# Performance work log

Hardware: AMD Instinct MI355X
Metric: run time of the kernel (lower is better)

## Reference

```python
import jax, jax.numpy as jnp
import numpy as np

# norse LIFParameters defaults
ALPHA = 100.0        # superspike surrogate slope
DT = 1e-3
TAU_SYN_INV = 200.0  # 1/5e-3
TAU_MEM_INV = 100.0  # 1/1e-2
V_TH = 1.0           # v_leak = v_reset = 0

@jax.custom_vjp
def heaviside(v):
    # forward: hard threshold; backward: superspike surrogate 1/(alpha*|v|+1)^2
    return (v > 0).astype(v.dtype)

def _hv_fwd(v):
    return heaviside(v), v

def _hv_bwd(v, g):
    return (g / (ALPHA * jnp.abs(v) + 1.0) ** 2,)

heaviside.defvjp(_hv_fwd, _hv_bwd)

def setup_inputs() -> dict:
    key = jax.random.key(0)
    ks = jax.random.split(key, 5)
    B, H, W, O = 2048, 15, 15, 10
    x = jax.random.uniform(ks[0], (B, 1, H, W), jnp.float32)  # image-like in [0,1)
    conv_w = jax.random.normal(ks[1], (2, 1, 4, 4), jnp.float32) * 0.25
    conv_b = jax.random.normal(ks[2], (2,), jnp.float32) * 0.1
    lin_w = jax.random.normal(ks[3], (O, 72), jnp.float32) * (1.0 / np.sqrt(72.0))
    lin_b = jax.random.normal(ks[4], (O,), jnp.float32) * 0.1
    return {"x": x, "conv_w": conv_w, "conv_b": conv_b,
            "lin_w": lin_w, "lin_b": lin_b, "num_steps": 300}

def reference(x, conv_w, conv_b, lin_w, lin_b, num_steps):
    B = x.shape[0]
    O = lin_w.shape[0]
    current = x * 10.0  # constant input current to the encoder

    def step(carry, _):
        v_enc, v, i = carry
        # --- constant_current_lif_encode step (lif_current_encoder) ---
        v_enc = v_enc + DT * TAU_MEM_INV * (-v_enc + current)
        z_in = heaviside(v_enc - V_TH)
        v_enc = v_enc - z_in * v_enc  # reset to v_reset = 0
        # --- feed-forward: conv -> maxpool(2) -> linear ---
        c = jax.lax.conv_general_dilated(
            z_in, conv_w, (1, 1), 'VALID',
            dimension_numbers=('NCHW', 'OIHW', 'NCHW')) + conv_b[None, :, None, None]
        p = jax.lax.reduce_window(c, -jnp.inf, jax.lax.max,
                                  (1, 1, 2, 2), (1, 1, 2, 2), 'VALID')  # [B,2,6,6]
        lin = p.reshape(B, -1) @ lin_w.T + lin_b  # [B,O]
        # --- norse LIFCell (lif_feed_forward_step) ---
        v_dec = v + DT * TAU_MEM_INV * (-v + i)
        i_dec = i - DT * TAU_SYN_INV * i
        spk = heaviside(v_dec - V_TH)
        v_new = (1.0 - spk) * v_dec  # v_reset = 0
        i_new = i_dec + lin
        return (v_enc, v_new, i_new), (spk, v_new)

    init = (jnp.zeros_like(current),
            jnp.zeros((B, O), x.dtype),
            jnp.zeros((B, O), x.dtype))
    _, (spk_rec, mem_rec) = jax.lax.scan(step, init, None, length=num_steps)
    spk_out = spk_rec.sum(0)  # [B,O]
    return spk_out, mem_rec, spk_rec
```

## Files before the change

kernel.cpp:

```cpp
#include <hip/hip_runtime.h>
#include <math.h>


typedef float v2f __attribute__((ext_vector_type(2)));
typedef unsigned long long u64;

#define DPPQ(x, ctrl) \
    __int_as_float(__builtin_amdgcn_mov_dpp(__float_as_int(x), (ctrl), 0xf, 0xf, true))

__global__ __launch_bounds__(256, 4) void snn_step_kernel(
    const float* __restrict__ x,
    const float* __restrict__ conv_w,
    const float* __restrict__ conv_b,
    const float* __restrict__ lin_w,
    const float* __restrict__ lin_b,
    float* __restrict__ out,
    int T, int B)
{
    const int b   = blockIdx.x;
    const int tid = threadIdx.x;
    const int w   = tid & 63;
    const int wv  = tid >> 6;

    __shared__ float4         s_lut[4][32];
    __shared__ unsigned short s_K[4][64];
    __shared__ float          s_p[4][2][80];
    __shared__ float          s_lin[300][10];

    if (tid < 128) {
        const int ky = tid >> 5, n = tid & 31;
        float s00 = 0.f, s01 = 0.f, s10 = 0.f, s11 = 0.f;
#pragma unroll
        for (int kx = 0; kx < 4; ++kx) {
            const float w0 = conv_w[ky * 4 + kx];
            const float w1 = conv_w[16 + ky * 4 + kx];
            if ((n >> kx) & 1)       { s00 += w0; s01 += w1; }
            if ((n >> (kx + 1)) & 1) { s10 += w0; s11 += w1; }
        }
        s_lut[ky][n] = make_float4(s00, s01, s10, s11);
    }

    {
        const int  row = 4 * wv + (w >> 4), col = w & 15;
        const bool act = (col < 15) && (row < 15);
        const float cur = act ? __fmul_rn(x[(size_t)b * 225 + row * 15 + col], 10.0f)
                              : 0.f;
        int   Kp = (cur > 1.0f) ? 0 : -1;
        float ve = 0.f;
        int t = 0;
        while (t < T) {
            if (__ballot(Kp == 0) == 0ull) break;
#pragma unroll
            for (int u = 0; u < 4; ++u) {
                float vn = __fadd_rn(ve, __fmul_rn(0.1f, __fsub_rn(cur, ve)));
                bool sp = (vn > 1.0f);
                Kp = (Kp == 0 && sp) ? (t + u + 1) : Kp;
                ve = sp ? 0.f : vn;
            }
            t += 4;
        }
        s_K[wv][w] = (unsigned short)(Kp > 0 ? Kp : 0);
    }
    __syncthreads();

    const bool convlane = (w < 36);
    const int  py = w / 6, px = w - 6 * py;
    const int  shx = 2 * px, shx16 = shx + 16;
    const int  poff = 20 * (w / 9) + 2 * (w - 9 * (w / 9));
    const v2f  cb2 = (v2f){conv_b[0], conv_b[1]};
    const bool qe0 = ((py >> 1) == 0), qe1 = ((py >> 1) == 1);
    const bool pyodd = (py & 1) != 0;

    const int lo = w >> 2, lq = w & 3;
    v2f lw2[9];
#pragma unroll
    for (int t = 0; t < 9; ++t) {
        int i0 = lo * 72 + 9 * lq + t;
        int i1 = i0 + 36;
        lw2[t] = (v2f){lin_w[i0 < 720 ? i0 : 719], lin_w[i1 < 720 ? i1 : 719]};
    }
    const float lbias = lin_b[lo < 10 ? lo : 0];

    const int Lc = T >> 2;
    const int t0 = wv * Lc;

    const int Ka = s_K[0][w], Kb = s_K[1][w], Kc = s_K[2][w], Kd = s_K[3][w];
    int ca = Ka ? (Ka - 1 - t0 % Ka) : 0x0FFFFFFF;
    int cb = Kb ? (Kb - 1 - t0 % Kb) : 0x0FFFFFFF;
    int cc = Kc ? (Kc - 1 - t0 % Kc) : 0x0FFFFFFF;
    int cd = Kd ? (Kd - 1 - t0 % Kd) : 0x0FFFFFFF;

    auto enc_words = [&](unsigned& wb0, unsigned& wb1, unsigned& wb2) {
        bool sp0 = (ca == 0); u64 b0 = __ballot(sp0); ca = sp0 ? (Ka - 1) : (ca - 1);
        bool sp1 = (cb == 0); u64 b1 = __ballot(sp1); cb = sp1 ? (Kb - 1) : (cb - 1);
        bool sp2 = (cc == 0); u64 b2 = __ballot(sp2); cc = sp2 ? (Kc - 1) : (cc - 1);
        bool sp3 = (cd == 0); u64 b3 = __ballot(sp3); cd = sp3 ? (Kd - 1) : (cd - 1);
        u64 balA = qe0 ? b0 : (qe1 ? b1 : b2);
        u64 balB = qe0 ? b1 : (qe1 ? b2 : b3);
        wb0 = pyodd ? (unsigned)(balA >> 32) : (unsigned)balA;
        wb1 = pyodd ? (unsigned)balB         : (unsigned)(balA >> 32);
        wb2 = pyodd ? (unsigned)(balB >> 32) : (unsigned)balB;
    };

    auto conv_compute = [&](int dbuf, unsigned wb0, unsigned wb1, unsigned wb2) {
        const int i0 = (wb0 >> shx)   & 31;
        const int i1 = (wb0 >> shx16) & 31;
        const int i2 = (wb1 >> shx)   & 31;
        const int i3 = (wb1 >> shx16) & 31;
        const int i4 = (wb2 >> shx)   & 31;

        const float4 f0 = s_lut[0][i0];
        const float4 f1 = s_lut[1][i1];
        const float4 f2 = s_lut[2][i2];
        const float4 f3 = s_lut[3][i3];
        const float4 g0 = s_lut[0][i1];
        const float4 g1 = s_lut[1][i2];
        const float4 g2 = s_lut[2][i3];
        const float4 g3 = s_lut[3][i4];

        v2f a00 = (v2f){f0.x, f0.y};  a00 += (v2f){f1.x, f1.y};
        a00 += (v2f){f2.x, f2.y};     a00 += (v2f){f3.x, f3.y};
        v2f a01 = (v2f){f0.z, f0.w};  a01 += (v2f){f1.z, f1.w};
        a01 += (v2f){f2.z, f2.w};     a01 += (v2f){f3.z, f3.w};
        v2f a10 = (v2f){g0.x, g0.y};  a10 += (v2f){g1.x, g1.y};
        a10 += (v2f){g2.x, g2.y};     a10 += (v2f){g3.x, g3.y};
        v2f a11 = (v2f){g0.z, g0.w};  a11 += (v2f){g1.z, g1.w};
        a11 += (v2f){g2.z, g2.w};     a11 += (v2f){g3.z, g3.w};

        v2f mraw = __builtin_elementwise_max(
                       __builtin_elementwise_max(a00, a01),
                       __builtin_elementwise_max(a10, a11));
        v2f m2 = mraw + cb2;

        *(v2f*)&s_p[wv][dbuf][poff] = m2;
    };

    auto lin_step = [&](int sm1) {
        const float* base = &s_p[wv][sm1 & 1][lq * 20];
        float4 q0 = *(const float4*)(base + 0);
        float4 q1 = *(const float4*)(base + 4);
        float4 q2 = *(const float4*)(base + 8);
        float4 q3 = *(const float4*)(base + 12);
        v2f    q4 = *(const v2f*)(base + 16);
        v2f pacc = (v2f){0.f, 0.f};
        pacc = __builtin_elementwise_fma(lw2[0], (v2f){q0.x, q0.y}, pacc);
        pacc = __builtin_elementwise_fma(lw2[1], (v2f){q0.z, q0.w}, pacc);
        pacc = __builtin_elementwise_fma(lw2[2], (v2f){q1.x, q1.y}, pacc);
        pacc = __builtin_elementwise_fma(lw2[3], (v2f){q1.z, q1.w}, pacc);
        pacc = __builtin_elementwise_fma(lw2[4], (v2f){q2.x, q2.y}, pacc);
        pacc = __builtin_elementwise_fma(lw2[5], (v2f){q2.z, q2.w}, pacc);
        pacc = __builtin_elementwise_fma(lw2[6], (v2f){q3.x, q3.y}, pacc);
        pacc = __builtin_elementwise_fma(lw2[7], (v2f){q3.z, q3.w}, pacc);
        pacc = __builtin_elementwise_fma(lw2[8], q4, pacc);
        float partial = __fadd_rn(pacc.x, pacc.y);

        float p1 = DPPQ(partial, 177);
        float p2 = DPPQ(partial, 78);
        float p3 = DPPQ(partial, 27);
        float lin = __fadd_rn(
            __fadd_rn(__fadd_rn(__fadd_rn(partial, p1), p2), p3), lbias);

        if (lq == 0 && lo < 10) s_lin[t0 + sm1][lo] = lin;
    };

    {
        unsigned wb0, wb1, wb2;
        enc_words(wb0, wb1, wb2);
        if (convlane) conv_compute(0, wb0, wb1, wb2);
    }
    for (int s = 1; s < Lc; ++s) {
        unsigned wb0, wb1, wb2;
        enc_words(wb0, wb1, wb2);
        if (convlane) conv_compute(s & 1, wb0, wb1, wb2);
        lin_step(s - 1);
    }
    lin_step(Lc - 1);
    __syncthreads();

    if (wv == 0) {
        float v = 0.f, i_syn = 0.f, sc = 0.f;
        const int o = (w < 10) ? w : 0;
        const size_t BO = (size_t)B * 10;
        float* mp  = out + BO + (size_t)b * 10 + o;
        float* spp = out + BO + (size_t)T * BO + (size_t)b * 10 + o;
#pragma unroll 4
        for (int t = 0; t < T; ++t) {
            float lv  = s_lin[t][o];
            float vd  = __fadd_rn(v, __fmul_rn(0.1f, __fsub_rn(i_syn, v)));
            float id  = __fsub_rn(i_syn, __fmul_rn(0.2f, i_syn));
            float spk = (vd > 1.0f) ? 1.0f : 0.0f;
            v = (vd > 1.0f) ? 0.0f : vd;
            sc += spk;
            i_syn = __fadd_rn(id, lv);
            if (w < 10) { *mp = v; *spp = spk; }
            mp  += BO;
            spp += BO;
        }
        if (w < 10) out[(size_t)b * 10 + w] = sc;
    }
}

extern "C" void kernel_launch(void* const* d_in, const int* in_sizes, int n_in,
                              void* d_out, int out_size, void* d_ws, size_t ws_size,
                              hipStream_t stream) {
    const float* x      = (const float*)d_in[0];
    const float* conv_w = (const float*)d_in[1];
    const float* conv_b = (const float*)d_in[2];
    const float* lin_w  = (const float*)d_in[3];
    const float* lin_b  = (const float*)d_in[4];
    float* out = (float*)d_out;

    const int B = in_sizes[0] / 225;
    const int T = (out_size / (B * 10) - 1) / 2;

    snn_step_kernel<<<B, 256, 0, stream>>>(x, conv_w, conv_b, lin_w, lin_b, out, T, B);
}
```

Baseline: 188.9 us.

## Build conv LUT once in a separate kernel and read it from global memory

The per-block construction of the 4x32 conv lookup table in shared memory is moved into a one-block pre-kernel that writes the table to workspace memory. The main kernel then reads the LUT through global (cached) loads instead of LDS, and the occupancy hint is raised from 4 to 8 blocks per SM. This removes redundant LUT setup per block and a little shared memory, but adds an extra kernel launch and turns fast LDS gathers in the hot conv loop into divergent global/L1 loads.

```diff
diff --git a/kernel.cpp b/kernel.cpp
--- a/kernel.cpp
+++ b/kernel.cpp
@@ -8,12 +8,28 @@
 #define DPPQ(x, ctrl) \
     __int_as_float(__builtin_amdgcn_mov_dpp(__float_as_int(x), (ctrl), 0xf, 0xf, true))
 
-__global__ __launch_bounds__(256, 4) void snn_step_kernel(
+__global__ __launch_bounds__(128, 1) void build_lut_kernel(
+    const float* __restrict__ conv_w, float4* __restrict__ lut_g)
+{
+    const int t  = threadIdx.x;
+    const int ky = t >> 5, n = t & 31;
+    float s00 = 0.f, s01 = 0.f, s10 = 0.f, s11 = 0.f;
+#pragma unroll
+    for (int kx = 0; kx < 4; ++kx) {
+        const float w0 = conv_w[ky * 4 + kx];
+        const float w1 = conv_w[16 + ky * 4 + kx];
+        if ((n >> kx) & 1)       { s00 += w0; s01 += w1; }
+        if ((n >> (kx + 1)) & 1) { s10 += w0; s11 += w1; }
+    }
+    lut_g[ky * 32 + n] = make_float4(s00, s01, s10, s11);
+}
+
+__global__ __launch_bounds__(256, 8) void snn_step_kernel(
     const float* __restrict__ x,
-    const float* __restrict__ conv_w,
     const float* __restrict__ conv_b,
     const float* __restrict__ lin_w,
     const float* __restrict__ lin_b,
+    const float4* __restrict__ glut,
     float* __restrict__ out,
     int T, int B)
 {
@@ -22,23 +38,9 @@
     const int w   = tid & 63;
     const int wv  = tid >> 6;
 
-    __shared__ float4         s_lut[4][32];
     __shared__ unsigned short s_K[4][64];
     __shared__ float          s_p[4][2][80];
     __shared__ float          s_lin[300][10];
-
-    if (tid < 128) {
-        const int ky = tid >> 5, n = tid & 31;
-        float s00 = 0.f, s01 = 0.f, s10 = 0.f, s11 = 0.f;
-#pragma unroll
-        for (int kx = 0; kx < 4; ++kx) {
-            const float w0 = conv_w[ky * 4 + kx];
-            const float w1 = conv_w[16 + ky * 4 + kx];
-            if ((n >> kx) & 1)       { s00 += w0; s01 += w1; }
-            if ((n >> (kx + 1)) & 1) { s10 += w0; s11 += w1; }
-        }
-        s_lut[ky][n] = make_float4(s00, s01, s10, s11);
-    }
 
     {
         const int  row = 4 * wv + (w >> 4), col = w & 15;
@@ -109,14 +111,14 @@
         const int i3 = (wb1 >> shx16) & 31;
         const int i4 = (wb2 >> shx)   & 31;
 
-        const float4 f0 = s_lut[0][i0];
-        const float4 f1 = s_lut[1][i1];
-        const float4 f2 = s_lut[2][i2];
-        const float4 f3 = s_lut[3][i3];
-        const float4 g0 = s_lut[0][i1];
-        const float4 g1 = s_lut[1][i2];
-        const float4 g2 = s_lut[2][i3];
-        const float4 g3 = s_lut[3][i4];
+        const float4 f0 = glut[i0];
+        const float4 f1 = glut[32 + i1];
+        const float4 f2 = glut[64 + i2];
+        const float4 f3 = glut[96 + i3];
+        const float4 g0 = glut[i1];
+        const float4 g1 = glut[32 + i2];
+        const float4 g2 = glut[64 + i3];
+        const float4 g3 = glut[96 + i4];
 
         v2f a00 = (v2f){f0.x, f0.y};  a00 += (v2f){f1.x, f1.y};
         a00 += (v2f){f2.x, f2.y};     a00 += (v2f){f3.x, f3.y};
@@ -213,5 +215,8 @@
     const int B = in_sizes[0] / 225;
     const int T = (out_size / (B * 10) - 1) / 2;
 
-    snn_step_kernel<<<B, 256, 0, stream>>>(x, conv_w, conv_b, lin_w, lin_b, out, T, B);
+    float4* lut_g = (float4*)d_ws;
+    build_lut_kernel<<<1, 128, 0, stream>>>(conv_w, lut_g);
+    snn_step_kernel<<<B, 256, 0, stream>>>(x, conv_b, lin_w, lin_b,
+                                           lut_g, out, T, B);
 }
```

Measured after the change: 297.3 us. +57.4%, slower.
